# Kernel tuning notes

Measured on AMD Instinct MI355X. Metric: run time of the kernel, lower is better.

Reference implementation:

```python
import jax, jax.numpy as jnp
import numpy as np

N_WIRES = 8
DIM = 1 << N_WIRES  # 256

# --- static precompute: CNOT-ring basis permutation and PauliZ sign matrix ---
# torchquantum convention: wire 0 is the most significant bit of the basis index.
_gates = [(w, w + 1) for w in range(N_WIRES - 1)] + [(N_WIRES - 1, 0)]
_perm = np.empty(DIM, dtype=np.int64)
for b in range(DIM):
    bits = [(b >> (N_WIRES - 1 - w)) & 1 for w in range(N_WIRES)]
    for c, t in _gates:
        if bits[c]:
            bits[t] ^= 1
    _perm[b] = sum(bit << (N_WIRES - 1 - w) for w, bit in enumerate(bits))
_Z = np.array([[1.0 - 2.0 * ((idx >> (N_WIRES - 1 - w)) & 1) for w in range(N_WIRES)]
               for idx in range(DIM)], dtype=np.float32)
# exp_Z[w] = sum_b probs_in[b] * Z[perm[b], w]  (CNOTs permute basis states)
_M = jnp.asarray(_Z[_perm])  # [256, 8]


def _quantum_head(angles):
    """angles: [..., 8] RX angles -> PauliZ expectations [..., 8].

    Circuit: RX(angle_w) on each wire from |0>, CNOT ring, MeasureAll(PauliZ).
    Post-RX state is a product state; CNOTs only permute basis states, so
    probabilities suffice (no complex amplitudes needed).
    """
    half = angles * 0.5
    c2 = jnp.cos(half) ** 2  # P(qubit=0)
    s2 = jnp.sin(half) ** 2  # P(qubit=1)
    # Build the 256-dim joint probability vector via sequential outer products.
    p = jnp.ones(angles.shape[:-1] + (1,), angles.dtype)
    for w in range(N_WIRES):
        pw = jnp.stack([c2[..., w], s2[..., w]], axis=-1)  # [..., 2]
        p = (p[..., :, None] * pw[..., None, :]).reshape(angles.shape[:-1] + (-1,))
    return p @ _M.astype(p.dtype)  # [..., 8]


def setup_inputs() -> dict:
    key = jax.random.key(0)
    ks = jax.random.split(key, 6)
    B, S, E = 8, 512, 768
    scale = 1.0 / np.sqrt(E)
    return {
        "x": jax.random.normal(ks[0], (B, S, E), jnp.float32),
        "W_proj": jax.random.normal(ks[1], (E, E), jnp.float32) * scale,
        "b_proj": jax.random.normal(ks[2], (E,), jnp.float32) * 0.02,
        "theta": jax.random.normal(ks[3], (N_WIRES,), jnp.float32),
        "W_comb": jax.random.normal(ks[4], (E, E), jnp.float32) * scale,
        "b_comb": jax.random.normal(ks[5], (E,), jnp.float32) * 0.02,
    }


def reference(x, W_proj, b_proj, theta, W_comb, b_comb):
    B, S, E = x.shape
    H = E // N_WIRES  # num_heads = 96
    proj = x @ W_proj.T + b_proj                 # [B, S, E] (torch Linear)
    angles = proj.reshape(B, S, H, N_WIRES) + theta  # encoder RX(x) then RX(theta): angles add
    expz = _quantum_head(angles)                 # [B, S, H, 8]
    out = expz.reshape(B, S, E)                  # heads re-concatenated
    # dropout is identity in eval mode
    return out @ W_comb.T + b_comb
```

## Files before the change

kernel.cpp:

```cpp
#include <hip/hip_runtime.h>

typedef _Float16 v8h __attribute__((ext_vector_type(8)));
typedef float    v4f __attribute__((ext_vector_type(4)));

__device__ __forceinline__ void gl_lds16(const void* g, void* l) {
  __builtin_amdgcn_global_load_lds(
      (__attribute__((address_space(1))) void*)(void*)g,
      (__attribute__((address_space(3))) void*)l, 16, 0, 0);
}

__global__ void conv_f16(const float4* __restrict__ in, v8h* __restrict__ out) {
  const int i = blockIdx.x * blockDim.x + threadIdx.x;
  const float4 a = in[2 * i];
  const float4 b = in[2 * i + 1];
  v8h o;
  o[0] = (_Float16)a.x; o[1] = (_Float16)a.y; o[2] = (_Float16)a.z; o[3] = (_Float16)a.w;
  o[4] = (_Float16)b.x; o[5] = (_Float16)b.y; o[6] = (_Float16)b.z; o[7] = (_Float16)b.w;
  out[i] = o;
}

__global__ __launch_bounds__(256) void gemm_f16(
    const _Float16* __restrict__ A, int lda,
    const _Float16* __restrict__ B, int ldb,
    float* __restrict__ C, int ldc,
    int K, const float* __restrict__ bias) {
  const int t = threadIdx.x;
  const int b = blockIdx.x;
  const int xcd = b & 7, slot = b >> 3;
  const int bm = xcd * 8 + slot / 12;
  const int bn = slot % 12;

  const int wave = t >> 6, lane = t & 63;
  const int quad = lane >> 4, l16 = lane & 15;
  const int wm = (wave >> 1) * 32, wn = (wave & 1) * 32;

  __shared__ __align__(16) _Float16 As[64 * 32];
  __shared__ __align__(16) _Float16 Bs[64 * 32];

  const int srow = t >> 2;
  const int scol = (t & 3) * 8;
  const _Float16* Ag = A + (size_t)(bm * 64 + srow) * lda + scol;
  const _Float16* Bg = B + (size_t)(bn * 64 + srow) * ldb + scol;
  _Float16* Al = &As[srow * 32 + scol];
  _Float16* Bl = &Bs[srow * 32 + scol];

  v4f acc[2][2];
#pragma unroll
  for (int i = 0; i < 2; i++)
#pragma unroll
    for (int j = 0; j < 2; j++) acc[i][j] = (v4f){0.f, 0.f, 0.f, 0.f};

  for (int kt = 0; kt < K; kt += 32) {
    gl_lds16(Ag + kt, Al);
    gl_lds16(Bg + kt, Bl);
    __syncthreads();
    v8h af[2], bf[2];
#pragma unroll
    for (int i = 0; i < 2; i++)
      af[i] = *(const v8h*)&As[(wm + i * 16 + l16) * 32 + quad * 8];
#pragma unroll
    for (int j = 0; j < 2; j++)
      bf[j] = *(const v8h*)&Bs[(wn + j * 16 + l16) * 32 + quad * 8];
#pragma unroll
    for (int i = 0; i < 2; i++)
#pragma unroll
      for (int j = 0; j < 2; j++)
        acc[i][j] = __builtin_amdgcn_mfma_f32_16x16x32_f16(af[i], bf[j], acc[i][j], 0, 0, 0);
    __syncthreads();
  }

  const int row0 = bm * 64 + wm + quad * 4;
  const int col0 = bn * 64 + wn + l16;
#pragma unroll
  for (int j = 0; j < 2; j++) {
    const int col = col0 + j * 16;
    const float bv = bias ? bias[col] : 0.f;
#pragma unroll
    for (int i = 0; i < 2; i++) {
#pragma unroll
      for (int r = 0; r < 4; r++) {
        C[(size_t)(row0 + i * 16 + r) * ldc + col] = acc[i][j][r] + bv;
      }
    }
  }
}

__global__ void quantum_head(const float* __restrict__ proj,
                             const float* __restrict__ b_proj,
                             const float* __restrict__ theta,
                             _Float16* __restrict__ EZ) {
  const int h = blockIdx.x * blockDim.x + threadIdx.x;
  const int token = h / 96;
  const int head = h - token * 96;
  const size_t off = (size_t)token * 768 + head * 8;
  const float4 p0 = *(const float4*)(proj + off);
  const float4 p1 = *(const float4*)(proj + off + 4);
  const float4 b0 = *(const float4*)(b_proj + head * 8);
  const float4 b1 = *(const float4*)(b_proj + head * 8 + 4);
  float c[8];
  c[0] = cosf(p0.x + b0.x + theta[0]);
  c[1] = cosf(p0.y + b0.y + theta[1]);
  c[2] = cosf(p0.z + b0.z + theta[2]);
  c[3] = cosf(p0.w + b0.w + theta[3]);
  c[4] = cosf(p1.x + b1.x + theta[4]);
  c[5] = cosf(p1.y + b1.y + theta[5]);
  c[6] = cosf(p1.z + b1.z + theta[6]);
  c[7] = cosf(p1.w + b1.w + theta[7]);
  float e[8];
  e[0] = c[1] * c[2] * c[3] * c[4] * c[5] * c[6] * c[7];
  float pr = c[0];
#pragma unroll
  for (int w = 1; w < 8; w++) { pr *= c[w]; e[w] = pr; }
  v8h ov;
#pragma unroll
  for (int w = 0; w < 8; w++) ov[w] = (_Float16)e[w];
  *(v8h*)(EZ + (size_t)h * 8) = ov;
}

extern "C" void kernel_launch(void* const* d_in, const int* in_sizes, int n_in,
                              void* d_out, int out_size, void* d_ws, size_t ws_size,
                              hipStream_t stream) {
  const float* x     = (const float*)d_in[0];
  const float* Wp    = (const float*)d_in[1];
  const float* bp    = (const float*)d_in[2];
  const float* theta = (const float*)d_in[3];
  const float* Wcf   = (const float*)d_in[4];
  const float* bc    = (const float*)d_in[5];
  float* out = (float*)d_out;

  const int M = 4096, E = 768;
  const size_t ME = (size_t)M * E;
  const size_t EE = (size_t)E * E;

  _Float16* XH  = (_Float16*)d_ws;
  _Float16* WPH = XH + ME;
  _Float16* WCH = WPH + EE;
  _Float16* EZ  = WCH + EE;
  float* proj   = (float*)(EZ + ME);

  conv_f16<<<(int)(ME / 8 / 256), 256, 0, stream>>>((const float4*)x, (v8h*)XH);
  conv_f16<<<(int)(EE / 8 / 256), 256, 0, stream>>>((const float4*)Wp, (v8h*)WPH);
  conv_f16<<<(int)(EE / 8 / 256), 256, 0, stream>>>((const float4*)Wcf, (v8h*)WCH);

  gemm_f16<<<768, 256, 0, stream>>>(XH, 768, WPH, 768, proj, 768, 768, nullptr);

  quantum_head<<<1536, 256, 0, stream>>>(proj, bp, theta, EZ);

  gemm_f16<<<768, 256, 0, stream>>>(EZ, 768, WCH, 768, out, 768, 768, bc);
}
```

Baseline: 116.7 us.

## Fuse x conversion and quantum head into first GEMM, merge weight conversions

The first GEMM now reads fp32 x directly, converts it to fp16 in registers and stores it to LDS, which removes the separate x conversion pass. The quantum-head math (bias, theta, cosines, products) runs in the GEMM epilogue from an LDS-staged C tile, so the fp32 proj intermediate and its kernel disappear. The two weight conversions are merged into one launch. In exchange, A-tile loads become synchronous register loads instead of async global-to-LDS copies, which may expose more latency inside the K loop.

Measured after the change: 111.5 us. -4.4%, faster.

```diff
diff --git a/kernel.cpp b/kernel.cpp
--- a/kernel.cpp
+++ b/kernel.cpp
@@ -9,14 +9,121 @@
       (__attribute__((address_space(3))) void*)l, 16, 0, 0);
 }
 
-__global__ void conv_f16(const float4* __restrict__ in, v8h* __restrict__ out) {
-  const int i = blockIdx.x * blockDim.x + threadIdx.x;
-  const float4 a = in[2 * i];
-  const float4 b = in[2 * i + 1];
+__global__ void conv_w(const float4* __restrict__ wp, const float4* __restrict__ wc,
+                       v8h* __restrict__ op, v8h* __restrict__ oc) {
+  const int n = 73728;
+  int i = blockIdx.x * blockDim.x + threadIdx.x;
+  const float4* src = (i < n) ? wp : wc;
+  v8h* dst = (i < n) ? op : oc;
+  const int j = (i < n) ? i : i - n;
+  const float4 a = src[2 * j];
+  const float4 b = src[2 * j + 1];
   v8h o;
   o[0] = (_Float16)a.x; o[1] = (_Float16)a.y; o[2] = (_Float16)a.z; o[3] = (_Float16)a.w;
   o[4] = (_Float16)b.x; o[5] = (_Float16)b.y; o[6] = (_Float16)b.z; o[7] = (_Float16)b.w;
-  out[i] = o;
+  dst[j] = o;
+}
+
+__global__ __launch_bounds__(256) void gemm1_qh(
+    const float* __restrict__ X,
+    const _Float16* __restrict__ B,
+    const float* __restrict__ bp,
+    const float* __restrict__ theta,
+    _Float16* __restrict__ EZ) {
+  const int t = threadIdx.x;
+  const int b = blockIdx.x;
+  const int xcd = b & 7, slot = b >> 3;
+  const int bm = xcd * 8 + slot / 12;
+  const int bn = slot % 12;
+
+  const int wave = t >> 6, lane = t & 63;
+  const int quad = lane >> 4, l16 = lane & 15;
+  const int wm = (wave >> 1) * 32, wn = (wave & 1) * 32;
+
+  __shared__ __align__(16) unsigned char smem[64 * 68 * 4];
+  _Float16* As = (_Float16*)smem;
+  _Float16* Bs = (_Float16*)(smem + 4096);
+  float* Cs = (float*)smem;
+
+  const float4 th0 = *(const float4*)theta;
+  const float4 th1 = *(const float4*)(theta + 4);
+
+  const int srow = t >> 2, sg = t & 3;
+  const float* Xg = X + (size_t)(bm * 64 + srow) * 768 + sg * 8;
+  const _Float16* Bg = B + (size_t)(bn * 64 + srow) * 768 + sg * 8;
+  _Float16* Al = &As[t * 8];
+  _Float16* Bl = &Bs[t * 8];
+
+  v4f acc[2][2];
+#pragma unroll
+  for (int i = 0; i < 2; i++)
+#pragma unroll
+    for (int j = 0; j < 2; j++) acc[i][j] = (v4f){0.f, 0.f, 0.f, 0.f};
+
+  for (int kt = 0; kt < 768; kt += 32) {
+    const float4 a0 = *(const float4*)(Xg + kt);
+    const float4 a1 = *(const float4*)(Xg + kt + 4);
+    gl_lds16(Bg + kt, Bl);
+    v8h av;
+    av[0] = (_Float16)a0.x; av[1] = (_Float16)a0.y; av[2] = (_Float16)a0.z; av[3] = (_Float16)a0.w;
+    av[4] = (_Float16)a1.x; av[5] = (_Float16)a1.y; av[6] = (_Float16)a1.z; av[7] = (_Float16)a1.w;
+    *(v8h*)Al = av;
+    __syncthreads();
+    v8h af[2], bf[2];
+#pragma unroll
+    for (int i = 0; i < 2; i++)
+      af[i] = *(const v8h*)&As[(wm + i * 16 + l16) * 32 + quad * 8];
+#pragma unroll
+    for (int j = 0; j < 2; j++)
+      bf[j] = *(const v8h*)&Bs[(wn + j * 16 + l16) * 32 + quad * 8];
+#pragma unroll
+    for (int i = 0; i < 2; i++)
+#pragma unroll
+      for (int j = 0; j < 2; j++)
+        acc[i][j] = __builtin_amdgcn_mfma_f32_16x16x32_f16(af[i], bf[j], acc[i][j], 0, 0, 0);
+    __syncthreads();
+  }
+
+  const int r0 = wm + quad * 4;
+  const int c0 = wn + l16;
+#pragma unroll
+  for (int j = 0; j < 2; j++)
+#pragma unroll
+    for (int i = 0; i < 2; i++)
+#pragma unroll
+      for (int r = 0; r < 4; r++)
+        Cs[(r0 + i * 16 + r) * 68 + c0 + j * 16] = acc[i][j][r];
+  __syncthreads();
+
+#pragma unroll
+  for (int s = 0; s < 2; s++) {
+    const int idx = t + s * 256;
+    const int row = idx >> 3, h = idx & 7;
+    const int gcol = bn * 64 + h * 8;
+    const float* cr = &Cs[row * 68 + h * 8];
+    const float4 q0 = *(const float4*)cr;
+    const float4 q1 = *(const float4*)(cr + 4);
+    const float4 b0 = *(const float4*)(bp + gcol);
+    const float4 b1 = *(const float4*)(bp + gcol + 4);
+    float c[8];
+    c[0] = cosf(q0.x + b0.x + th0.x);
+    c[1] = cosf(q0.y + b0.y + th0.y);
+    c[2] = cosf(q0.z + b0.z + th0.z);
+    c[3] = cosf(q0.w + b0.w + th0.w);
+    c[4] = cosf(q1.x + b1.x + th1.x);
+    c[5] = cosf(q1.y + b1.y + th1.y);
+    c[6] = cosf(q1.z + b1.z + th1.z);
+    c[7] = cosf(q1.w + b1.w + th1.w);
+    float e[8];
+    e[0] = c[1] * c[2] * c[3] * c[4] * c[5] * c[6] * c[7];
+    float pr = c[0];
+#pragma unroll
+    for (int w = 1; w < 8; w++) { pr *= c[w]; e[w] = pr; }
+    v8h ov;
+#pragma unroll
+    for (int w = 0; w < 8; w++) ov[w] = (_Float16)e[w];
+    *(v8h*)(EZ + (size_t)(bm * 64 + row) * 768 + gcol) = ov;
+  }
 }
 
 __global__ __launch_bounds__(256) void gemm_f16(
@@ -85,38 +192,6 @@
   }
 }
 
-__global__ void quantum_head(const float* __restrict__ proj,
-                             const float* __restrict__ b_proj,
-                             const float* __restrict__ theta,
-                             _Float16* __restrict__ EZ) {
-  const int h = blockIdx.x * blockDim.x + threadIdx.x;
-  const int token = h / 96;
-  const int head = h - token * 96;
-  const size_t off = (size_t)token * 768 + head * 8;
-  const float4 p0 = *(const float4*)(proj + off);
-  const float4 p1 = *(const float4*)(proj + off + 4);
-  const float4 b0 = *(const float4*)(b_proj + head * 8);
-  const float4 b1 = *(const float4*)(b_proj + head * 8 + 4);
-  float c[8];
-  c[0] = cosf(p0.x + b0.x + theta[0]);
-  c[1] = cosf(p0.y + b0.y + theta[1]);
-  c[2] = cosf(p0.z + b0.z + theta[2]);
-  c[3] = cosf(p0.w + b0.w + theta[3]);
-  c[4] = cosf(p1.x + b1.x + theta[4]);
-  c[5] = cosf(p1.y + b1.y + theta[5]);
-  c[6] = cosf(p1.z + b1.z + theta[6]);
-  c[7] = cosf(p1.w + b1.w + theta[7]);
-  float e[8];
-  e[0] = c[1] * c[2] * c[3] * c[4] * c[5] * c[6] * c[7];
-  float pr = c[0];
-#pragma unroll
-  for (int w = 1; w < 8; w++) { pr *= c[w]; e[w] = pr; }
-  v8h ov;
-#pragma unroll
-  for (int w = 0; w < 8; w++) ov[w] = (_Float16)e[w];
-  *(v8h*)(EZ + (size_t)h * 8) = ov;
-}
-
 extern "C" void kernel_launch(void* const* d_in, const int* in_sizes, int n_in,
                               void* d_out, int out_size, void* d_ws, size_t ws_size,
                               hipStream_t stream) {
@@ -132,19 +207,14 @@
   const size_t ME = (size_t)M * E;
   const size_t EE = (size_t)E * E;
 
-  _Float16* XH  = (_Float16*)d_ws;
-  _Float16* WPH = XH + ME;
+  _Float16* WPH = (_Float16*)d_ws;
   _Float16* WCH = WPH + EE;
   _Float16* EZ  = WCH + EE;
-  float* proj   = (float*)(EZ + ME);
-
-  conv_f16<<<(int)(ME / 8 / 256), 256, 0, stream>>>((const float4*)x, (v8h*)XH);
-  conv_f16<<<(int)(EE / 8 / 256), 256, 0, stream>>>((const float4*)Wp, (v8h*)WPH);
-  conv_f16<<<(int)(EE / 8 / 256), 256, 0, stream>>>((const float4*)Wcf, (v8h*)WCH);
-
-  gemm_f16<<<768, 256, 0, stream>>>(XH, 768, WPH, 768, proj, 768, 768, nullptr);
-
-  quantum_head<<<1536, 256, 0, stream>>>(proj, bp, theta, EZ);
+
+  conv_w<<<(int)(2 * EE / 8 / 256), 256, 0, stream>>>(
+      (const float4*)Wp, (const float4*)Wcf, (v8h*)WPH, (v8h*)WCH);
+
+  gemm1_qh<<<768, 256, 0, stream>>>(x, WPH, bp, theta, EZ);
 
   gemm_f16<<<768, 256, 0, stream>>>(EZ, 768, WCH, 768, out, 768, 768, bc);
 }
```
